# Optimization experiments

Hardware: AMD Instinct MI355X
Metric: run time of the kernel (lower is better)

Reference implementation:

```python
import jax, jax.numpy as jnp
import numpy as np

B, NQ, NP_, D = 4, 2048, 8192, 256
T, H = 10, 4  # num_tables, num_hash_functions -> hash code length T*H = 40


def setup_inputs() -> dict:
    key = jax.random.key(0)
    k1, k2, k3 = jax.random.split(key, 3)
    return {
        "query_points": jax.random.normal(k1, (B, NQ, D), dtype=jnp.float32),
        "points": jax.random.normal(k2, (B, NP_, D), dtype=jnp.float32),
        "proj": jax.random.normal(k3, (T * H, D), dtype=jnp.float32),  # projection_matrices
        "k": 16,
    }


def _hash(x, proj):
    # x: [B, N, D], proj: [T*H, D] -> binary hash [B, N, T*H]
    return (jnp.einsum('bnd,fd->bnf', x, proj) > 0).astype(jnp.float32)


def reference(query_points, points, proj, k):
    qh = _hash(query_points, proj)   # [B, Nq, F]
    ph = _hash(points, proj)         # [B, Np, F]
    # L1 cdist on {0,1}-valued vectors == Hamming: |a-b| = a + b - 2ab (exact in fp32).
    sq = qh.sum(-1)                  # [B, Nq]
    sp = ph.sum(-1)                  # [B, Np]
    dist = sq[:, :, None] + sp[:, None, :] - 2.0 * jnp.einsum('bqf,bpf->bqp', qh, ph)
    kk = min(int(k), points.shape[1])
    neg_vals, indices = jax.lax.top_k(-dist, kk)  # smallest-k distances
    return indices, -neg_vals
```

## Files before the change

kernel.cpp:

```cpp
#include <hip/hip_runtime.h>
#include <stdint.h>

#define B_  4
#define NQ_ 2048
#define NP_ 8192
#define D_  256
#define F_  40
#define K_  16

__global__ __launch_bounds__(256) void hash_kernel(
    const float* __restrict__ qp, const float* __restrict__ pp,
    const float* __restrict__ proj, uint64_t* __restrict__ qcodes,
    uint64_t* __restrict__ pcodes) {
  __shared__ float tile[64 * 257];
  int t = threadIdx.x;
  int v0 = blockIdx.x * 64;
  bool isQ = v0 < B_ * NQ_;
  const float* src =
      isQ ? (qp + (size_t)v0 * D_) : (pp + (size_t)(v0 - B_ * NQ_) * D_);

#pragma unroll 8
  for (int i = 0; i < 64; ++i) tile[i * 257 + t] = src[i * 256 + t];
  __syncthreads();

  int lane = t & 63, w = t >> 6;
  int fbase = __builtin_amdgcn_readfirstlane(w * 10);
  const float* pj = proj + (size_t)fbase * 256;

  float acc[10];
#pragma unroll
  for (int f = 0; f < 10; ++f) acc[f] = 0.0f;
#pragma unroll 4
  for (int d = 0; d < 256; ++d) {
    float x = tile[lane * 257 + d];
#pragma unroll
    for (int f = 0; f < 10; ++f) acc[f] = fmaf(x, pj[f * 256 + d], acc[f]);
  }
  unsigned bits = 0;
#pragma unroll
  for (int f = 0; f < 10; ++f)
    if (acc[f] > 0.0f) bits |= 1u << f;

  __syncthreads();
  unsigned short* cb = (unsigned short*)tile;
  cb[lane * 4 + w] = (unsigned short)bits;
  __syncthreads();
  if (w == 0) {
    uint64_t code = (uint64_t)cb[lane * 4 + 0] |
                    ((uint64_t)cb[lane * 4 + 1] << 10) |
                    ((uint64_t)cb[lane * 4 + 2] << 20) |
                    ((uint64_t)cb[lane * 4 + 3] << 30);
    int gv = v0 + lane;
    if (isQ) qcodes[gv] = code;
    else pcodes[gv - B_ * NQ_] = code;
  }
}

__global__ __launch_bounds__(1024) void select_kernel(
    const uint64_t* __restrict__ qcodes, const uint64_t* __restrict__ pcodes,
    float* __restrict__ outIdx, float* __restrict__ outDist) {
  __shared__ ulonglong2 ldsP2[NP_ / 2];
  __shared__ unsigned keybuf[16][K_];
  uint64_t* ldsP = (uint64_t*)ldsP2;

  int tid = threadIdx.x;
  int bb = blockIdx.x >> 7;
  const ulonglong2* pb2 = (const ulonglong2*)(pcodes + (size_t)bb * NP_);
  for (int i = tid; i < NP_ / 2; i += 1024) ldsP2[i] = pb2[i];
  __syncthreads();

  int w = tid >> 6, lane = tid & 63;
  int qg = blockIdx.x * 16 + w;
  uint64_t qc = qcodes[qg];
  const uint64_t M = 0x00FF00FF00FF00FFull;

  unsigned nb = 0;
  uint64_t cf = 0;
#pragma unroll 4
  for (int j = 0; j < 64; ++j) {
    ulonglong2 pc = ldsP2[j * 64 + lane];
    unsigned d0 = (unsigned)__popcll(qc ^ pc.x);
    unsigned d1 = (unsigned)__popcll(qc ^ pc.y);
    nb += (d0 < 8u) + (d1 < 8u);
    unsigned r0 = d0 - 8u, r1 = d1 - 8u;
    uint64_t a0 = (r0 < 8u) ? (1ull << (r0 << 3)) : 0ull;
    uint64_t a1 = (r1 < 8u) ? (1ull << (r1 << 3)) : 0ull;
    cf += a0 + a1;
  }
  uint64_t e = cf & M, o = (cf >> 8) & M;
#pragma unroll
  for (int s = 1; s < 64; s <<= 1) {
    e += __shfl_xor(e, s);
    o += __shfl_xor(o, s);
    nb += __shfl_xor(nb, s);
  }

  int t = 0;
  unsigned n_lt = 0;
  bool ok = false;
  if (nb < (unsigned)K_) {
    unsigned cum = nb;
#pragma unroll
    for (int r = 0; r < 8; ++r) {
      unsigned c = (unsigned)(((r & 1) ? o : e) >> ((r >> 1) * 16)) & 0xFFFFu;
      if (!ok && cum + c >= K_) { t = 8 + r; n_lt = cum; ok = true; }
      cum += c;
    }
  }

  if (!ok) {
    uint64_t c8 = 0;
#pragma unroll 4
    for (int j = 0; j < 64; ++j) {
      ulonglong2 pc = ldsP2[j * 64 + lane];
      int d0 = __popcll(qc ^ pc.x);
      int d1 = __popcll(qc ^ pc.y);
      c8 += (1ull << (d0 & 56)) + (1ull << (d1 & 56));
    }
    uint64_t e2 = c8 & M, o2 = (c8 >> 8) & M;
#pragma unroll
    for (int s = 1; s < 64; s <<= 1) {
      e2 += __shfl_xor(e2, s);
      o2 += __shfl_xor(o2, s);
    }
    int Bb = 0;
    unsigned nbefore = 0, cum = 0;
    bool found = false;
#pragma unroll
    for (int k2 = 0; k2 < 6; ++k2) {
      unsigned c = (unsigned)(((k2 & 1) ? o2 : e2) >> ((k2 >> 1) * 16)) & 0xFFFFu;
      if (!found && cum + c >= K_) { Bb = k2; nbefore = cum; found = true; }
      cum += c;
    }
    int base = Bb * 8;
    uint64_t cff = 0;
#pragma unroll 4
    for (int j = 0; j < 64; ++j) {
      ulonglong2 pc = ldsP2[j * 64 + lane];
      unsigned r0 = (unsigned)(__popcll(qc ^ pc.x) - base);
      unsigned r1 = (unsigned)(__popcll(qc ^ pc.y) - base);
      if (r0 < 8u) cff += 1ull << (r0 << 3);
      if (r1 < 8u) cff += 1ull << (r1 << 3);
    }
    uint64_t ef = cff & M, of = (cff >> 8) & M;
#pragma unroll
    for (int s = 1; s < 64; s <<= 1) {
      ef += __shfl_xor(ef, s);
      of += __shfl_xor(of, s);
    }
    unsigned cum2 = nbefore;
    bool f2 = false;
#pragma unroll
    for (int r = 0; r < 8; ++r) {
      unsigned c = (unsigned)(((r & 1) ? of : ef) >> ((r >> 1) * 16)) & 0xFFFFu;
      if (!f2 && cum2 + c >= K_) { t = base + r; n_lt = cum2; f2 = true; }
      cum2 += c;
    }
  }
  unsigned r_need = K_ - n_lt;

  unsigned cl = 0, ce = 0;
  uint64_t lmask = (1ull << lane) - 1;
  for (int j = 0; j < 128; ++j) {
    int p = j * 64 + lane;
    int d = __popcll(qc ^ ldsP[p]);
    if (__any(d <= t)) {
      bool blt = (d < t), beq = (d == t);
      uint64_t mlt = __ballot(blt), meq = __ballot(beq);
      if (blt)
        keybuf[w][cl + (unsigned)__popcll(mlt & lmask)] =
            ((unsigned)d << 13) | (unsigned)p;
      if (beq) {
        unsigned pos = ce + (unsigned)__popcll(meq & lmask);
        if (pos < r_need)
          keybuf[w][n_lt + pos] = ((unsigned)d << 13) | (unsigned)p;
      }
      cl += (unsigned)__popcll(mlt);
      ce += (unsigned)__popcll(meq);
    }
  }
  __syncthreads();

  if (lane < K_) {
    unsigned my = keybuf[w][lane];
    int rank = 0;
#pragma unroll
    for (int jj = 0; jj < K_; ++jj) rank += (keybuf[w][jj] < my) ? 1 : 0;
    int off = qg * K_ + rank;
    outIdx[off]  = (float)(my & 8191u);
    outDist[off] = (float)(my >> 13);
  }
}

extern "C" void kernel_launch(void* const* d_in, const int* in_sizes, int n_in,
                              void* d_out, int out_size, void* d_ws, size_t ws_size,
                              hipStream_t stream) {
  const float* qp   = (const float*)d_in[0];
  const float* pp   = (const float*)d_in[1];
  const float* proj = (const float*)d_in[2];

  uint64_t* pcodes = (uint64_t*)d_ws;
  uint64_t* qcodes = pcodes + (size_t)B_ * NP_;

  float* outIdx  = (float*)d_out;
  float* outDist = outIdx + (size_t)B_ * NQ_ * K_;

  int total_vecs = B_ * (NQ_ + NP_);
  hash_kernel<<<total_vecs / 64, 256, 0, stream>>>(qp, pp, proj, qcodes, pcodes);
  select_kernel<<<B_ * NQ_ / 16, 1024, 0, stream>>>(qcodes, pcodes, outIdx, outDist);
}
```

Before: 162.8 us.

## Cache clamped Hamming distances in registers to skip LDS rescan in fast path

During the first histogram pass, each lane packs its 128 Hamming distances, clamped to 4 bits, into 16 registers. The histogram is clamped into the [8,15] buckets so no separate below-8 count is needed. When the threshold falls in buckets 9..14, the selection pass reads distances from these registers instead of reloading codes from LDS and recomputing popcounts, and it handles two candidates per ballot step. This cuts LDS traffic and popcount work in the common case, at the cost of more registers, full unrolling with sched barriers, and more ballots per iteration. Ordering of the selected points changes but is fixed by the later rank sort.

```diff
diff --git a/kernel.cpp b/kernel.cpp
--- a/kernel.cpp
+++ b/kernel.cpp
@@ -74,41 +74,81 @@
   uint64_t qc = qcodes[qg];
   const uint64_t M = 0x00FF00FF00FF00FFull;
 
-  unsigned nb = 0;
+  unsigned pack[16];
+#pragma unroll
+  for (int i = 0; i < 16; ++i) pack[i] = 0;
   uint64_t cf = 0;
-#pragma unroll 4
-  for (int j = 0; j < 64; ++j) {
-    ulonglong2 pc = ldsP2[j * 64 + lane];
+#pragma unroll
+  for (int j2 = 0; j2 < 64; ++j2) {
+    ulonglong2 pc = ldsP2[j2 * 64 + lane];
     unsigned d0 = (unsigned)__popcll(qc ^ pc.x);
     unsigned d1 = (unsigned)__popcll(qc ^ pc.y);
-    nb += (d0 < 8u) + (d1 < 8u);
-    unsigned r0 = d0 - 8u, r1 = d1 - 8u;
-    uint64_t a0 = (r0 < 8u) ? (1ull << (r0 << 3)) : 0ull;
-    uint64_t a1 = (r1 < 8u) ? (1ull << (r1 << 3)) : 0ull;
-    cf += a0 + a1;
+    unsigned c0 = d0 < 15u ? d0 : 15u;
+    unsigned c1 = d1 < 15u ? d1 : 15u;
+    pack[j2 >> 2] |= (c0 << (((2 * j2) & 7) * 4)) | (c1 << (((2 * j2 + 1) & 7) * 4));
+    int r0 = (int)d0 - 8; r0 = r0 < 0 ? 0 : (r0 > 7 ? 7 : r0);
+    int r1 = (int)d1 - 8; r1 = r1 < 0 ? 0 : (r1 > 7 ? 7 : r1);
+    cf += (1ull << (r0 << 3)) + (1ull << (r1 << 3));
+    if ((j2 & 7) == 7) __builtin_amdgcn_sched_barrier(0);
   }
   uint64_t e = cf & M, o = (cf >> 8) & M;
 #pragma unroll
   for (int s = 1; s < 64; s <<= 1) {
     e += __shfl_xor(e, s);
     o += __shfl_xor(o, s);
-    nb += __shfl_xor(nb, s);
   }
 
   int t = 0;
   unsigned n_lt = 0;
-  bool ok = false;
-  if (nb < (unsigned)K_) {
-    unsigned cum = nb;
+  int rfound = -1;
+  {
+    unsigned cum = 0;
 #pragma unroll
     for (int r = 0; r < 8; ++r) {
       unsigned c = (unsigned)(((r & 1) ? o : e) >> ((r >> 1) * 16)) & 0xFFFFu;
-      if (!ok && cum + c >= K_) { t = 8 + r; n_lt = cum; ok = true; }
+      if (rfound < 0 && cum + c >= K_) { rfound = r; t = 8 + r; n_lt = cum; }
       cum += c;
     }
   }
-
-  if (!ok) {
+  uint64_t lmask = (1ull << lane) - 1;
+
+  if (rfound >= 1 && rfound <= 6) {
+    unsigned r_need = K_ - n_lt;
+    unsigned cl = 0, ce = 0;
+    unsigned ut = (unsigned)t;
+#pragma unroll
+    for (int j2 = 0; j2 < 64; ++j2) {
+      unsigned pw = pack[j2 >> 2];
+      unsigned d0 = (pw >> (((2 * j2) & 7) * 4)) & 0xFu;
+      unsigned d1 = (pw >> (((2 * j2 + 1) & 7) * 4)) & 0xFu;
+      int p0 = j2 * 128 + 2 * lane;
+      uint64_t m0 = __ballot(d0 < ut);
+      uint64_t m1 = __ballot(d1 < ut);
+      if (m0 | m1) {
+        unsigned base =
+            cl + (unsigned)__popcll(m0 & lmask) + (unsigned)__popcll(m1 & lmask);
+        if (d0 < ut) keybuf[w][base] = (d0 << 13) | (unsigned)p0;
+        if (d1 < ut)
+          keybuf[w][base + (unsigned)((m0 >> lane) & 1)] =
+              (d1 << 13) | (unsigned)(p0 + 1);
+        cl += (unsigned)__popcll(m0) + (unsigned)__popcll(m1);
+      }
+      if (ce < r_need) {
+        uint64_t q0 = __ballot(d0 == ut);
+        uint64_t q1 = __ballot(d1 == ut);
+        if (q0 | q1) {
+          unsigned b2 =
+              ce + (unsigned)__popcll(q0 & lmask) + (unsigned)__popcll(q1 & lmask);
+          unsigned pos1 = b2 + (unsigned)((q0 >> lane) & 1);
+          if (d0 == ut && b2 < r_need)
+            keybuf[w][n_lt + b2] = (ut << 13) | (unsigned)p0;
+          if (d1 == ut && pos1 < r_need)
+            keybuf[w][n_lt + pos1] = (ut << 13) | (unsigned)(p0 + 1);
+          ce += (unsigned)__popcll(q0) + (unsigned)__popcll(q1);
+        }
+      }
+    }
+  } else {
     uint64_t c8 = 0;
 #pragma unroll 4
     for (int j = 0; j < 64; ++j) {
@@ -156,27 +196,25 @@
       if (!f2 && cum2 + c >= K_) { t = base + r; n_lt = cum2; f2 = true; }
       cum2 += c;
     }
-  }
-  unsigned r_need = K_ - n_lt;
-
-  unsigned cl = 0, ce = 0;
-  uint64_t lmask = (1ull << lane) - 1;
-  for (int j = 0; j < 128; ++j) {
-    int p = j * 64 + lane;
-    int d = __popcll(qc ^ ldsP[p]);
-    if (__any(d <= t)) {
-      bool blt = (d < t), beq = (d == t);
-      uint64_t mlt = __ballot(blt), meq = __ballot(beq);
-      if (blt)
-        keybuf[w][cl + (unsigned)__popcll(mlt & lmask)] =
-            ((unsigned)d << 13) | (unsigned)p;
-      if (beq) {
-        unsigned pos = ce + (unsigned)__popcll(meq & lmask);
-        if (pos < r_need)
-          keybuf[w][n_lt + pos] = ((unsigned)d << 13) | (unsigned)p;
+    unsigned r_need = K_ - n_lt;
+    unsigned cl = 0, ce = 0;
+    for (int j = 0; j < 128; ++j) {
+      int p = j * 64 + lane;
+      int d = __popcll(qc ^ ldsP[p]);
+      if (__any(d <= t)) {
+        bool blt = (d < t), beq = (d == t);
+        uint64_t mlt = __ballot(blt), meq = __ballot(beq);
+        if (blt)
+          keybuf[w][cl + (unsigned)__popcll(mlt & lmask)] =
+              ((unsigned)d << 13) | (unsigned)p;
+        if (beq) {
+          unsigned pos = ce + (unsigned)__popcll(meq & lmask);
+          if (pos < r_need)
+            keybuf[w][n_lt + pos] = ((unsigned)d << 13) | (unsigned)p;
+        }
+        cl += (unsigned)__popcll(mlt);
+        ce += (unsigned)__popcll(meq);
       }
-      cl += (unsigned)__popcll(mlt);
-      ce += (unsigned)__popcll(meq);
     }
   }
   __syncthreads();
```

After: 163.0 us. About the same (+0.1%).
